# Kernel optimization log

Hardware: AMD Instinct MI355X
Metric: run time of the kernel (lower is better)

The kernel has to match this reference:

```python
import jax, jax.numpy as jnp
import numpy as np


def setup_inputs() -> dict:
    key = jax.random.key(0)
    k1, k2 = jax.random.split(key)
    B, N, M, D = 4, 8192, 8192, 3
    pred_points = jax.random.normal(k1, (B, N, D), dtype=jnp.float32)
    gt_points = jax.random.normal(k2, (B, M, D), dtype=jnp.float32)
    return {"pred_points": pred_points, "gt_points": gt_points}


def reference(pred_points, gt_points):
    p2 = jnp.sum(pred_points * pred_points, axis=-1)  # [B, N]
    g2 = jnp.sum(gt_points * gt_points, axis=-1)      # [B, M]
    cross = jnp.einsum("bnd,bmd->bnm", pred_points, gt_points)  # [B, N, M]
    d2 = p2[:, :, None] + g2[:, None, :] - 2.0 * cross
    dist = jnp.sqrt(jnp.maximum(d2, 0.0))             # [B, N, M]
    min_pred_to_gt = jnp.min(dist, axis=-1)           # [B, N]
    min_gt_to_pred = jnp.min(dist, axis=-2)           # [B, M]
    return min_pred_to_gt.mean() + min_gt_to_pred.mean()
```

## Files before the change

### kernel.cpp

```cpp
#include <hip/hip_runtime.h>


#define B_ 4
#define N_ 8192
#define QPT 8
#define THREADS 256
#define S_ 32
#define TT (N_ / S_)

__device__ __forceinline__ float min3f(float a, float b, float c) {
  float d;
  asm("v_min3_f32 %0, %1, %2, %3" : "=v"(d) : "v"(a), "v"(b), "v"(c));
  return d;
}

__global__ __launch_bounds__(THREADS) void chamfer_min2(
    const float* __restrict__ pred, const float* __restrict__ gt,
    float* __restrict__ partial, float* __restrict__ accws) {
  __shared__ float4 sh[TT];

  const int tid = threadIdx.x;
  const int dirb = blockIdx.z;
  const int dir = dirb >> 2;
  const int b = dirb & 3;

  if (blockIdx.x == 0 && blockIdx.y == 0 && blockIdx.z == 0 && tid < 2)
    ((unsigned*)accws)[tid] = 0u;

  const float* qsrc = (dir == 0 ? pred : gt) + (size_t)b * N_ * 3;
  const float* tsrc = (dir == 0 ? gt : pred) + (size_t)b * N_ * 3;

  {
    const float* tb = tsrc + (size_t)blockIdx.y * TT * 3;
    const float x = tb[3 * tid], y = tb[3 * tid + 1], z = tb[3 * tid + 2];
    sh[tid] = make_float4(x, y, z, fmaf(x, x, fmaf(y, y, z * z)));
  }
  __syncthreads();

  const int qbase = blockIdx.x * (THREADS * QPT) + tid;
  float nx[QPT], ny[QPT], nz[QPT], q2[QPT], acc[QPT];
#pragma unroll
  for (int k = 0; k < QPT; ++k) {
    const int qi = qbase + k * THREADS;
    const float x = qsrc[3 * qi], y = qsrc[3 * qi + 1], z = qsrc[3 * qi + 2];
    nx[k] = -2.0f * x; ny[k] = -2.0f * y; nz[k] = -2.0f * z;
    q2[k] = fmaf(x, x, fmaf(y, y, z * z));
    acc[k] = 3.4e38f;
  }

  for (int j0 = 0; j0 < TT; j0 += 16) {
#pragma unroll
    for (int jj = 0; jj < 16; jj += 2) {
      const float4 t0 = sh[j0 + jj];
      const float4 t1 = sh[j0 + jj + 1];
#pragma unroll
      for (int k = 0; k < QPT; ++k) {
        const float s0 = fmaf(nx[k], t0.x, fmaf(ny[k], t0.y, fmaf(nz[k], t0.z, t0.w)));
        const float s1 = fmaf(nx[k], t1.x, fmaf(ny[k], t1.y, fmaf(nz[k], t1.z, t1.w)));
        acc[k] = min3f(acc[k], s0, s1);
      }
    }
  }

  float* dst = partial + ((size_t)dirb * S_ + blockIdx.y) * N_;
#pragma unroll
  for (int k = 0; k < QPT; ++k) {
    const int qi = qbase + k * THREADS;
    dst[qi] = fmaxf(q2[k] + acc[k], 0.0f);
  }
}

__global__ __launch_bounds__(256) void chamfer_fin(
    const float* __restrict__ partial, float* __restrict__ accws,
    float* __restrict__ out) {
  const int t = blockIdx.x * 256 + threadIdx.x;
  const int base = t * 4;
  const int dirb = base >> 13;
  const int qi = base & (N_ - 1);

  const float4* p = (const float4*)(partial + (size_t)dirb * S_ * N_ + qi);
  const int stride4 = N_ / 4;
  float4 m = p[0];
#pragma unroll
  for (int s = 1; s < S_; s += 2) {
    const float4 a = p[(size_t)s * stride4];
    const float4 c = p[(size_t)(s + 1 < S_ ? s + 1 : s) * stride4];
    m.x = min3f(m.x, a.x, c.x);
    m.y = min3f(m.y, a.y, c.y);
    m.z = min3f(m.z, a.z, c.z);
    m.w = min3f(m.w, a.w, c.w);
  }
  float sum = sqrtf(m.x) + sqrtf(m.y) + sqrtf(m.z) + sqrtf(m.w);

#pragma unroll
  for (int off = 32; off > 0; off >>= 1) sum += __shfl_down(sum, off, 64);
  __shared__ float ws4[4];
  const int lane = threadIdx.x & 63, wid = threadIdx.x >> 6;
  if (lane == 0) ws4[wid] = sum;
  __syncthreads();
  if (threadIdx.x == 0) {
    const float bs = (ws4[0] + ws4[1]) + (ws4[2] + ws4[3]);
    atomicAdd(&accws[0], bs);
    __threadfence();
    const unsigned old = atomicAdd(((unsigned*)accws) + 1, 1u);
    if (old == gridDim.x - 1) {
      __threadfence();
      const float tot = atomicAdd(&accws[0], 0.0f);
      out[0] = tot * (1.0f / 32768.0f);
    }
  }
}

extern "C" void kernel_launch(void* const* d_in, const int* in_sizes, int n_in,
                              void* d_out, int out_size, void* d_ws, size_t ws_size,
                              hipStream_t stream) {
  const float* pred = (const float*)d_in[0];
  const float* gt   = (const float*)d_in[1];
  float* out = (float*)d_out;

  float* accws = (float*)d_ws;
  float* partial = (float*)((char*)d_ws + 64);

  chamfer_min2<<<dim3(N_ / (THREADS * QPT), S_, 2 * B_), THREADS, 0, stream>>>(
      pred, gt, partial, accws);
  chamfer_fin<<<64, 256, 0, stream>>>(partial, accws, out);
}
```

Baseline: 100.7 us.

## Compute squared distances with bf16 split-precision MFMA instead of scalar FMA

Replaces the scalar FP32 FMA distance loop with MFMA 32x32x16 bf16 matrix ops. Points are pre-packed into hi/lo bf16 splits, with norms folded into the K dimension, so one MFMA yields the full squared distance. Each block now covers the whole target set for a 64-row panel and writes row minima directly, which removes the 32-way partial-min buffer and shrinks the finish kernel. It adds a packing kernel and relies on the bf16 hi/lo split for accuracy, where cancellation in the norm expansion could introduce error.

New measurement: 87.60 us. -13.0%, faster.

```diff
diff --git a/kernel.cpp b/kernel.cpp
--- a/kernel.cpp
+++ b/kernel.cpp
@@ -3,95 +3,122 @@
 
 #define B_ 4
 #define N_ 8192
-#define QPT 8
-#define THREADS 256
-#define S_ 32
-#define TT (N_ / S_)
+#define THREADS 512
 
-__device__ __forceinline__ float min3f(float a, float b, float c) {
-  float d;
-  asm("v_min3_f32 %0, %1, %2, %3" : "=v"(d) : "v"(a), "v"(b), "v"(c));
-  return d;
+typedef float f32x16 __attribute__((ext_vector_type(16)));
+typedef short short8 __attribute__((ext_vector_type(8)));
+typedef unsigned short ushort8 __attribute__((ext_vector_type(8)));
+
+__device__ __forceinline__ unsigned short f2bf(float x) {
+  unsigned u = __float_as_uint(x);
+  u = u + 0x7FFFu + ((u >> 16) & 1u);
+  return (unsigned short)(u >> 16);
+}
+__device__ __forceinline__ float bf2f(unsigned short h) {
+  return __uint_as_float(((unsigned)h) << 16);
 }
 
-__global__ __launch_bounds__(THREADS) void chamfer_min2(
+__global__ __launch_bounds__(256) void chamfer_pack(
     const float* __restrict__ pred, const float* __restrict__ gt,
-    float* __restrict__ partial, float* __restrict__ accws) {
-  __shared__ float4 sh[TT];
+    unsigned short* __restrict__ Apack, unsigned short* __restrict__ Bpack,
+    float* __restrict__ accws) {
+  const int i = blockIdx.x * 256 + threadIdx.x;
+  if (i < 2) ((unsigned*)accws)[i] = 0u;
+  const int half = B_ * N_;
+  const float* src = (i < half) ? pred : gt;
+  const int k = (i < half) ? i : i - half;
+  const float x = src[3 * k], y = src[3 * k + 1], z = src[3 * k + 2];
+  const float q2 = fmaf(x, x, fmaf(y, y, z * z));
 
+  const float ux = -2.f * x, uy = -2.f * y, uz = -2.f * z;
+  const unsigned short uhx = f2bf(ux), uhy = f2bf(uy), uhz = f2bf(uz);
+  const unsigned short ulx = f2bf(ux - bf2f(uhx));
+  const unsigned short uly = f2bf(uy - bf2f(uhy));
+  const unsigned short ulz = f2bf(uz - bf2f(uhz));
+  const unsigned short thx = f2bf(x), thy = f2bf(y), thz = f2bf(z);
+  const unsigned short tlx = f2bf(x - bf2f(thx));
+  const unsigned short tly = f2bf(y - bf2f(thy));
+  const unsigned short tlz = f2bf(z - bf2f(thz));
+  const unsigned short q2h = f2bf(q2);
+  const unsigned short q2l = f2bf(q2 - bf2f(q2h));
+  const unsigned short one = 0x3F80u;
+
+  const size_t aslot = (size_t)i;
+  const size_t bslot = (size_t)((i < half) ? i + half : i - half);
+
+  ushort8 alo = {uhx, uhy, uhz, uhx, uhy, uhz, ulx, uly};
+  ushort8 ahi = {ulz, q2h, q2l, one, one, 0, 0, 0};
+  ushort8 blo = {thx, thy, thz, tlx, tly, tlz, thx, thy};
+  ushort8 bhi = {thz, one, one, q2h, q2l, 0, 0, 0};
+  *(ushort8*)(Apack + aslot * 16) = alo;
+  *(ushort8*)(Apack + aslot * 16 + 8) = ahi;
+  *(ushort8*)(Bpack + bslot * 16) = blo;
+  *(ushort8*)(Bpack + bslot * 16 + 8) = bhi;
+}
+
+__global__ __launch_bounds__(THREADS, 4) void chamfer_mfma(
+    const unsigned short* __restrict__ Apack,
+    const unsigned short* __restrict__ Bpack,
+    float* __restrict__ rowmin) {
+  __shared__ unsigned rowlds[64];
   const int tid = threadIdx.x;
-  const int dirb = blockIdx.z;
-  const int dir = dirb >> 2;
-  const int b = dirb & 3;
+  const int dirb = blockIdx.y;
+  const int panel = blockIdx.x;
+  const int w = tid >> 6, l = tid & 63;
+  const int wr = w >> 2, wc = w & 3;
+  const int l31 = l & 31, lhi = l >> 5;
 
-  if (blockIdx.x == 0 && blockIdx.y == 0 && blockIdx.z == 0 && tid < 2)
-    ((unsigned*)accws)[tid] = 0u;
+  if (tid < 64) rowlds[tid] = 0x7F7FFFFFu;
+  __syncthreads();
 
-  const float* qsrc = (dir == 0 ? pred : gt) + (size_t)b * N_ * 3;
-  const float* tsrc = (dir == 0 ? gt : pred) + (size_t)b * N_ * 3;
+  const int row = panel * 64 + wr * 32 + l31;
+  const short8 afrag =
+      *(const short8*)(Apack + ((size_t)dirb * N_ + row) * 16 + lhi * 8);
 
-  {
-    const float* tb = tsrc + (size_t)blockIdx.y * TT * 3;
-    const float x = tb[3 * tid], y = tb[3 * tid + 1], z = tb[3 * tid + 2];
-    sh[tid] = make_float4(x, y, z, fmaf(x, x, fmaf(y, y, z * z)));
+  const unsigned short* bp =
+      Bpack + ((size_t)dirb * N_ + wc * 32 + l31) * 16 + lhi * 8;
+
+  const f32x16 zacc = {};
+  float racc[16];
+#pragma unroll
+  for (int r = 0; r < 16; ++r) racc[r] = 3.4e38f;
+
+#pragma unroll 2
+  for (int step = 0; step < 64; ++step) {
+    const short8 bfrag = *(const short8*)(bp + (size_t)step * 128 * 16);
+    const f32x16 d =
+        __builtin_amdgcn_mfma_f32_32x32x16_bf16(afrag, bfrag, zacc, 0, 0, 0);
+#pragma unroll
+    for (int r = 0; r < 16; ++r) racc[r] = fminf(racc[r], d[r]);
+  }
+
+#pragma unroll
+  for (int r = 0; r < 16; ++r) racc[r] = fmaxf(racc[r], 0.0f);
+#pragma unroll
+  for (int m = 1; m <= 16; m <<= 1)
+#pragma unroll
+    for (int r = 0; r < 16; ++r)
+      racc[r] = fminf(racc[r], __shfl_xor(racc[r], m, 64));
+
+  if (l31 == 0) {
+#pragma unroll
+    for (int r = 0; r < 16; ++r) {
+      const int lr = wr * 32 + (r & 3) + 8 * (r >> 2) + 4 * lhi;
+      atomicMin(&rowlds[lr], __float_as_uint(racc[r]));
+    }
   }
   __syncthreads();
-
-  const int qbase = blockIdx.x * (THREADS * QPT) + tid;
-  float nx[QPT], ny[QPT], nz[QPT], q2[QPT], acc[QPT];
-#pragma unroll
-  for (int k = 0; k < QPT; ++k) {
-    const int qi = qbase + k * THREADS;
-    const float x = qsrc[3 * qi], y = qsrc[3 * qi + 1], z = qsrc[3 * qi + 2];
-    nx[k] = -2.0f * x; ny[k] = -2.0f * y; nz[k] = -2.0f * z;
-    q2[k] = fmaf(x, x, fmaf(y, y, z * z));
-    acc[k] = 3.4e38f;
-  }
-
-  for (int j0 = 0; j0 < TT; j0 += 16) {
-#pragma unroll
-    for (int jj = 0; jj < 16; jj += 2) {
-      const float4 t0 = sh[j0 + jj];
-      const float4 t1 = sh[j0 + jj + 1];
-#pragma unroll
-      for (int k = 0; k < QPT; ++k) {
-        const float s0 = fmaf(nx[k], t0.x, fmaf(ny[k], t0.y, fmaf(nz[k], t0.z, t0.w)));
-        const float s1 = fmaf(nx[k], t1.x, fmaf(ny[k], t1.y, fmaf(nz[k], t1.z, t1.w)));
-        acc[k] = min3f(acc[k], s0, s1);
-      }
-    }
-  }
-
-  float* dst = partial + ((size_t)dirb * S_ + blockIdx.y) * N_;
-#pragma unroll
-  for (int k = 0; k < QPT; ++k) {
-    const int qi = qbase + k * THREADS;
-    dst[qi] = fmaxf(q2[k] + acc[k], 0.0f);
-  }
+  if (tid < 64)
+    rowmin[(size_t)dirb * N_ + panel * 64 + tid] = __uint_as_float(rowlds[tid]);
 }
 
 __global__ __launch_bounds__(256) void chamfer_fin(
-    const float* __restrict__ partial, float* __restrict__ accws,
+    const float* __restrict__ rowmin, float* __restrict__ accws,
     float* __restrict__ out) {
   const int t = blockIdx.x * 256 + threadIdx.x;
-  const int base = t * 4;
-  const int dirb = base >> 13;
-  const int qi = base & (N_ - 1);
-
-  const float4* p = (const float4*)(partial + (size_t)dirb * S_ * N_ + qi);
-  const int stride4 = N_ / 4;
-  float4 m = p[0];
-#pragma unroll
-  for (int s = 1; s < S_; s += 2) {
-    const float4 a = p[(size_t)s * stride4];
-    const float4 c = p[(size_t)(s + 1 < S_ ? s + 1 : s) * stride4];
-    m.x = min3f(m.x, a.x, c.x);
-    m.y = min3f(m.y, a.y, c.y);
-    m.z = min3f(m.z, a.z, c.z);
-    m.w = min3f(m.w, a.w, c.w);
-  }
-  float sum = sqrtf(m.x) + sqrtf(m.y) + sqrtf(m.z) + sqrtf(m.w);
-
+  const float4 v = ((const float4*)rowmin)[t];
+  float sum = sqrtf(fmaxf(v.x, 0.f)) + sqrtf(fmaxf(v.y, 0.f)) +
+              sqrtf(fmaxf(v.z, 0.f)) + sqrtf(fmaxf(v.w, 0.f));
 #pragma unroll
   for (int off = 32; off > 0; off >>= 1) sum += __shfl_down(sum, off, 64);
   __shared__ float ws4[4];
@@ -119,9 +146,11 @@
   float* out = (float*)d_out;
 
   float* accws = (float*)d_ws;
-  float* partial = (float*)((char*)d_ws + 64);
+  unsigned short* Apack = (unsigned short*)((char*)d_ws + 64);
+  unsigned short* Bpack = Apack + (size_t)2 * B_ * N_ * 16;
+  float* rowmin = (float*)(Bpack + (size_t)2 * B_ * N_ * 16);
 
-  chamfer_min2<<<dim3(N_ / (THREADS * QPT), S_, 2 * B_), THREADS, 0, stream>>>(
-      pred, gt, partial, accws);
-  chamfer_fin<<<64, 256, 0, stream>>>(partial, accws, out);
+  chamfer_pack<<<256, 256, 0, stream>>>(pred, gt, Apack, Bpack, accws);
+  chamfer_mfma<<<dim3(128, 8), THREADS, 0, stream>>>(Apack, Bpack, rowmin);
+  chamfer_fin<<<64, 256, 0, stream>>>(rowmin, accws, out);
 }
```
